# Kernel tuning notes

Hardware: AMD Instinct MI355X
Metric: run time of the kernel (lower is better)

The kernel has to match this reference:

```python
import jax, jax.numpy as jnp
import numpy as np

B, T, C_IN, C_HID, C_EMB, K, MAX_DUR = 16, 512, 512, 256, 384, 5, 8
MAX_MEL = T * MAX_DUR  # static upper bound on regulated length (4096)
LRELU_SLOPE = 0.3
PAD = (K - 1) // 2
EPS = 1e-5


def setup_inputs() -> dict:
    key = jax.random.key(0)
    ks = jax.random.split(key, 14)
    s = 0.05
    return {
        "x": jax.random.normal(ks[0], (B, T, C_IN), jnp.float32),
        "x_res": jax.random.normal(ks[1], (B, T, C_IN), jnp.float32),
        "duration_target": jax.random.randint(ks[2], (B, T), 0, MAX_DUR, dtype=jnp.int32),
        "embeddings": jax.random.normal(ks[3], (B, T, C_EMB), jnp.float32),
        "src_mask": jnp.zeros((B, T), jnp.bool_),
        "conv1_w": s * jax.random.normal(ks[4], (K, C_IN, C_HID), jnp.float32),
        "conv1_b": jnp.zeros((C_HID,), jnp.float32),
        "ln1_g": jnp.ones((C_HID,), jnp.float32),
        "ln1_b": jnp.zeros((C_HID,), jnp.float32),
        "conv2_w": s * jax.random.normal(ks[5], (K, C_HID, C_HID), jnp.float32),
        "conv2_b": jnp.zeros((C_HID,), jnp.float32),
        "ln2_g": jnp.ones((C_HID,), jnp.float32),
        "ln2_b": jnp.zeros((C_HID,), jnp.float32),
        "lin_w": s * jax.random.normal(ks[6], (C_HID, 1), jnp.float32),
        "lin_b": jnp.zeros((1,), jnp.float32),
    }


def _conv1d(x, w, b):
    # x: [B, T, Cin], w: [K, Cin, Cout] -> [B, T, Cout] (same padding)
    y = jax.lax.conv_general_dilated(
        x, w, window_strides=(1,), padding=[(PAD, PAD)],
        dimension_numbers=("NWC", "WIO", "NWC"))
    return y + b


def _layer_norm(x, g, b):
    mu = jnp.mean(x, axis=-1, keepdims=True)
    var = jnp.mean(jnp.square(x - mu), axis=-1, keepdims=True)
    return (x - mu) * jax.lax.rsqrt(var + EPS) * g + b


def _duration_predictor(x, mask, c1w, c1b, g1, b1, c2w, c2b, g2, b2, lw, lb):
    h = jax.nn.leaky_relu(_conv1d(x, c1w, c1b), LRELU_SLOPE)
    h = _layer_norm(h, g1, b1)  # dropout is identity at eval
    h = jax.nn.leaky_relu(_conv1d(h, c2w, c2b), LRELU_SLOPE)
    h = _layer_norm(h, g2, b2)
    h = (h @ lw + lb).squeeze(-1)  # [B, T]
    return jnp.where(mask, 0.0, h)


def _length_regulate(x, duration):
    # Fused prefix-sum + gather replacement for the looped expand/cat/pad.
    # token i occupies output frames [cumsum[i-1], cumsum[i])
    cum = jnp.cumsum(duration, axis=1)              # [B, T]
    total = cum[:, -1]                              # [B] mel lengths
    pos = jnp.arange(MAX_MEL, dtype=cum.dtype)      # [MAX_MEL]
    idx = jax.vmap(lambda c: jnp.searchsorted(c, pos, side="right"))(cum)  # [B, MAX_MEL]
    idx = jnp.clip(idx, 0, duration.shape[1] - 1)
    valid = (pos[None, :] < total[:, None])         # [B, MAX_MEL]
    out = jnp.take_along_axis(x, idx[..., None], axis=1)
    out = out * valid[..., None].astype(x.dtype)    # zero-padded past mel_len
    return out, total.astype(jnp.int32)


def reference(x, x_res, duration_target, embeddings, src_mask,
              conv1_w, conv1_b, ln1_g, ln1_b, conv2_w, conv2_b, ln2_g, ln2_b,
              lin_w, lin_b):
    # upsample_train path: x_res is detached before the duration predictor
    x_res = jax.lax.stop_gradient(x_res)
    log_duration_prediction = _duration_predictor(
        x_res, src_mask, conv1_w, conv1_b, ln1_g, ln1_b,
        conv2_w, conv2_b, ln2_g, ln2_b, lin_w, lin_b)
    x_up, _ = _length_regulate(x, duration_target)
    emb_up, _ = _length_regulate(embeddings, duration_target)
    return x_up, log_duration_prediction, emb_up
```

## Files before the change

### kernel.cpp

```cpp
#include <hip/hip_runtime.h>


constexpr int Bn = 16, Tn = 512, CIN1 = 512, CHID = 256, CEMB = 384, MAXMEL = 4096;
constexpr int NROWS = Bn * Tn;
#define LRELU 0.3f
#define EPSV 1e-5f

typedef __attribute__((ext_vector_type(8))) short bf16x8;
typedef __attribute__((ext_vector_type(4))) float f32x4;
typedef __attribute__((ext_vector_type(16))) float f32x16;
typedef __attribute__((ext_vector_type(4))) unsigned int u32x4;
typedef unsigned short ushort_t;

static __device__ __forceinline__ ushort_t f2bf(float f) {
  unsigned u = __builtin_bit_cast(unsigned, f);
  unsigned r = (u + 0x7fffu + ((u >> 16) & 1u)) >> 16;
  return (ushort_t)r;
}

template <int CI, bool F32IN>
static __device__ __forceinline__ void conv_body(
    int mt, int ns,
    const float* __restrict__ xin, const ushort_t* __restrict__ inbf,
    const ushort_t* __restrict__ wB, float* __restrict__ hraw) {
  constexpr int NCHUNK = CI / 128;
  constexpr int ROWS = 36, LDSTRIDE = 136;
  __shared__ ushort_t sA[ROWS * LDSTRIDE];

  const int b = mt >> 4, t0 = (mt & 15) * 32;
  const int tid = threadIdx.x;
  const int l = tid & 63, nh = tid >> 6;
  const int lm = l & 31, lq = l >> 5;
  const int cob32 = ns * 4 + nh;

  f32x16 acc;
#pragma unroll
  for (int i = 0; i < 16; ++i) acc[i] = 0.f;

  const ushort_t* pB = wB + (size_t)cob32 * 512 + l * 8;

#pragma unroll 1
  for (int chunk = 0; chunk < NCHUNK; ++chunk) {
    {
      const int cibase = chunk * 128;
#pragma unroll 1
      for (int i = 0; i < 9; ++i) {
        const int p = i * 256 + tid;
        const int r = p >> 6, c2 = (p & 63) * 2;
        const int t = t0 - 2 + r;
        unsigned hv = 0;
        if ((unsigned)t < (unsigned)Tn) {
          const size_t src = (size_t)(b * Tn + t) * CI + cibase + c2;
          if (F32IN) {
            const float2 v = *(const float2*)(xin + src);
            hv = (unsigned)f2bf(v.x) | ((unsigned)f2bf(v.y) << 16);
          } else {
            hv = *(const unsigned*)(inbf + src);
          }
        }
        const int sw = ((r >> 3) & 3) << 3;
        *(unsigned*)&sA[r * LDSTRIDE + (c2 ^ sw)] = hv;
      }
    }
    __syncthreads();

#pragma unroll 1
    for (int ksh = 0; ksh < 5; ++ksh) {
      const int r = lm + ksh;
      const int sw = ((r >> 3) & 3) << 3;
      const size_t bbase = (size_t)((ksh * (CI / 16) + chunk * 8) * 8) * 512;
#pragma unroll
      for (int kk = 0; kk < 8; ++kk) {
        const int c = (kk * 16 + lq * 8) ^ sw;
        const bf16x8 a = *(const bf16x8*)&sA[r * LDSTRIDE + c];
        const bf16x8 bv = *(const bf16x8*)(pB + bbase + (size_t)kk * 8 * 512);
        acc = __builtin_amdgcn_mfma_f32_32x32x16_bf16(a, bv, acc, 0, 0, 0);
      }
    }
    __syncthreads();
  }

  const int col = ns * 128 + nh * 32 + lm;
  float* pOut = hraw + (size_t)(b * Tn + t0) * 256 + col;
#pragma unroll
  for (int reg = 0; reg < 16; ++reg) {
    const int row = (reg & 3) + 8 * (reg >> 2) + 4 * lq;
    pOut[(size_t)row * 256] = acc[reg];
  }
}

__global__ __launch_bounds__(256, 2) void conv1_gather_kernel(
    const float* __restrict__ x_res, const ushort_t* __restrict__ w1,
    float* __restrict__ hraw,
    const float* __restrict__ x, const int* __restrict__ idx,
    float* __restrict__ x_up) {
  const int blk = blockIdx.x;
  if (blk % 3 == 0) {
    const int cid = blk / 3;
    conv_body<512, true>(cid & 255, cid >> 8, x_res, nullptr, w1, hraw);
    return;
  }
  const int gid = blk - 1 - blk / 3;
  const f32x4* x4 = (const f32x4*)x;
  f32x4* xu4 = (f32x4*)x_up;
  const int tid0 = gid * 256 + threadIdx.x;
  const int stride = 1024 * 256;
  const f32x4 z = (f32x4){0.f, 0.f, 0.f, 0.f};
  for (int u = tid0; u < Bn * MAXMEL * 128; u += stride) {
    const int bp = u >> 7, i = u & 127;
    const int t = idx[bp];
    const int b = bp >> 12;
    const f32x4 v = (t >= 0) ? x4[((b << 9) + t) * 128 + i] : z;
    __builtin_nontemporal_store(v, &xu4[u]);
  }
}

__global__ __launch_bounds__(256, 2) void conv2_gather_kernel(
    const ushort_t* __restrict__ h1, const ushort_t* __restrict__ w2,
    float* __restrict__ hraw,
    const float* __restrict__ emb, const int* __restrict__ idx,
    float* __restrict__ emb_up) {
  const int blk = blockIdx.x;
  if (blk % 3 == 0) {
    const int cid = blk / 3;
    conv_body<256, false>(cid & 255, cid >> 8, nullptr, h1, w2, hraw);
    return;
  }
  const int gid = blk - 1 - blk / 3;
  const f32x4* e4 = (const f32x4*)emb;
  f32x4* eu4 = (f32x4*)emb_up;
  const int tid0 = gid * 256 + threadIdx.x;
  const int stride = 1024 * 256;
  const f32x4 z = (f32x4){0.f, 0.f, 0.f, 0.f};
  for (int u = tid0; u < Bn * MAXMEL * 96; u += stride) {
    const int bp = u / 96, i = u - bp * 96;
    const int t = idx[bp];
    const int b = bp >> 12;
    const f32x4 v = (t >= 0) ? e4[((b << 9) + t) * 96 + i] : z;
    __builtin_nontemporal_store(v, &eu4[u]);
  }
}

template <bool FINAL>
__global__ __launch_bounds__(256) void ln_kernel(
    const float* __restrict__ hraw,
    const float* __restrict__ bias, const float* __restrict__ g,
    const float* __restrict__ be, ushort_t* __restrict__ h1,
    const float* __restrict__ lw, const float* __restrict__ lb,
    const unsigned char* __restrict__ mask, float* __restrict__ ldp) {
  const int row = blockIdx.x * 4 + (threadIdx.x >> 6);
  const int l = threadIdx.x & 63;
  const f32x4 p = ((const f32x4*)hraw)[row * 64 + l];
  const f32x4 bi = ((const f32x4*)bias)[l];
  float v0 = p.x + bi.x, v1 = p.y + bi.y, v2 = p.z + bi.z, v3 = p.w + bi.w;
  v0 = (v0 > 0.f) ? v0 : LRELU * v0;
  v1 = (v1 > 0.f) ? v1 : LRELU * v1;
  v2 = (v2 > 0.f) ? v2 : LRELU * v2;
  v3 = (v3 > 0.f) ? v3 : LRELU * v3;
  float s = v0 + v1 + v2 + v3;
  float s2 = v0 * v0 + v1 * v1 + v2 * v2 + v3 * v3;
#pragma unroll
  for (int off = 32; off >= 1; off >>= 1) {
    s += __shfl_xor(s, off);
    s2 += __shfl_xor(s2, off);
  }
  const float mu = s * (1.f / 256.f);
  const float var = s2 * (1.f / 256.f) - mu * mu;
  const float rs = rsqrtf(var + EPSV);
  const f32x4 gg = ((const f32x4*)g)[l];
  const f32x4 bb = ((const f32x4*)be)[l];
  const float h0 = (v0 - mu) * rs * gg.x + bb.x;
  const float h1v = (v1 - mu) * rs * gg.y + bb.y;
  const float h2 = (v2 - mu) * rs * gg.z + bb.z;
  const float h3 = (v3 - mu) * rs * gg.w + bb.w;
  if (!FINAL) {
    ushort4 uh;
    uh.x = f2bf(h0); uh.y = f2bf(h1v); uh.z = f2bf(h2); uh.w = f2bf(h3);
    ((ushort4*)h1)[row * 64 + l] = uh;
  } else {
    const f32x4 lv = ((const f32x4*)lw)[l];
    float d = h0 * lv.x + h1v * lv.y + h2 * lv.z + h3 * lv.w;
#pragma unroll
    for (int off = 32; off >= 1; off >>= 1) d += __shfl_xor(d, off);
    if (l == 0) {
      float val = d + lb[0];
      if (mask[row]) val = 0.f;
      ldp[row] = val;
    }
  }
}

__global__ __launch_bounds__(512) void prep_kernel(
    const float* __restrict__ w1src, const float* __restrict__ w2src,
    ushort_t* __restrict__ w1dst, ushort_t* __restrict__ w2dst,
    const int* __restrict__ dur, int* __restrict__ idx) {
  __shared__ int wsum[8];
  const int blk = blockIdx.x;
  const int tid = threadIdx.x;
  if (blk < 240) {
    const float* src;
    ushort_t* dst;
    int CI, fr, sh;
    const int wv = tid >> 6, l = tid & 63;
    if (blk < 160) { src = w1src; dst = w1dst; CI = 512; sh = 5; fr = blk * 8 + wv; }
    else           { src = w2src; dst = w2dst; CI = 256; sh = 4; fr = (blk - 160) * 8 + wv; }
    const int cob32 = fr & 7;
    const int t = fr >> 3;
    const int ksh = t >> sh;
    const int ci16 = t & ((1 << sh) - 1);
    const int ci = ci16 * 16 + (l >> 5) * 8;
    const int co = cob32 * 32 + (l & 31);
    ushort_t v[8];
#pragma unroll
    for (int j = 0; j < 8; ++j)
      v[j] = f2bf(src[((size_t)(ksh * CI + ci + j)) * 256 + co]);
    u32x4 pack;
#pragma unroll
    for (int q = 0; q < 4; ++q)
      pack[q] = (unsigned)v[q * 2] | ((unsigned)v[q * 2 + 1] << 16);
    *(u32x4*)&dst[(size_t)fr * 512 + l * 8] = pack;
    return;
  }
  const int b = blk - 240;
  const int lane = tid & 63, wv = tid >> 6;
  const int d = dur[b * Tn + tid];
  int v = d;
#pragma unroll
  for (int off = 1; off <= 32; off <<= 1) {
    const int t = __shfl_up(v, off);
    if (lane >= off) v += t;
  }
  if (lane == 63) wsum[wv] = v;
  __syncthreads();
  int woff = 0, total = 0;
#pragma unroll
  for (int i = 0; i < 8; ++i) {
    const int s = wsum[i];
    if (i < wv) woff += s;
    total += s;
  }
  const int end = v + woff;
  for (int p = end - d; p < end; ++p) idx[b * MAXMEL + p] = tid;
  for (int p = total + tid; p < MAXMEL; p += 512) idx[b * MAXMEL + p] = -1;
}

extern "C" void kernel_launch(void* const* d_in, const int* in_sizes, int n_in,
                              void* d_out, int out_size, void* d_ws, size_t ws_size,
                              hipStream_t stream) {
  const float* x     = (const float*)d_in[0];
  const float* x_res = (const float*)d_in[1];
  const int*   dur   = (const int*)d_in[2];
  const float* emb   = (const float*)d_in[3];
  const unsigned char* mask = (const unsigned char*)d_in[4];
  const float* c1w = (const float*)d_in[5];
  const float* c1b = (const float*)d_in[6];
  const float* g1  = (const float*)d_in[7];
  const float* b1  = (const float*)d_in[8];
  const float* c2w = (const float*)d_in[9];
  const float* c2b = (const float*)d_in[10];
  const float* g2  = (const float*)d_in[11];
  const float* b2  = (const float*)d_in[12];
  const float* lw  = (const float*)d_in[13];
  const float* lb  = (const float*)d_in[14];

  float* x_up   = (float*)d_out;
  float* ldp    = x_up + (size_t)Bn * MAXMEL * CIN1;
  float* emb_up = ldp + (size_t)Bn * Tn;

  int* idx = (int*)d_ws;
  ushort_t* h1 = (ushort_t*)((char*)d_ws + (size_t)Bn * MAXMEL * 4);
  ushort_t* w1 = h1 + (size_t)NROWS * 256;
  ushort_t* w2 = w1 + (size_t)5 * 512 * 256;
  float* hraw = (float*)(w2 + (size_t)5 * 256 * 256);

  prep_kernel<<<256, 512, 0, stream>>>(c1w, c2w, w1, w2, dur, idx);
  conv1_gather_kernel<<<1536, 256, 0, stream>>>(
      x_res, w1, hraw, x, idx, x_up);
  ln_kernel<false><<<NROWS / 4, 256, 0, stream>>>(
      hraw, c1b, g1, b1, h1, nullptr, nullptr, nullptr, nullptr);
  conv2_gather_kernel<<<1536, 256, 0, stream>>>(
      h1, w2, hraw, emb, idx, emb_up);
  ln_kernel<true><<<NROWS / 4, 256, 0, stream>>>(
      hraw, c2b, g2, b2, nullptr, lw, lb, mask, ldp);
}
```

Baseline: 349.6 us.

## Fuse bias, LeakyReLU and LayerNorm into conv kernels with double-buffered staging

Each conv block now covers all 256 output channels with 512 threads, so the LayerNorm epilogue (and for conv2 the final linear projection plus mask) can run in-block through shuffle and shared-memory reductions. This removes the two standalone LN kernels and the fp32 hraw round trip through global memory. The A-tile staging is double-buffered, with the next chunk's global loads issued before the MFMA loop of the current chunk. Gather blocks grow to 512 threads with fewer blocks. Trade-offs are fewer conv blocks (256 instead of 512), higher register and LDS pressure per block, and extra syncs.

```diff
diff --git a/kernel.cpp b/kernel.cpp
--- a/kernel.cpp
+++ b/kernel.cpp
@@ -18,93 +18,200 @@
   return (ushort_t)r;
 }
 
-template <int CI, bool F32IN>
-static __device__ __forceinline__ void conv_body(
-    int mt, int ns,
+template <int CI, bool F32IN, bool FINAL>
+static __device__ __forceinline__ void conv_ln_body(
+    const int mt,
     const float* __restrict__ xin, const ushort_t* __restrict__ inbf,
-    const ushort_t* __restrict__ wB, float* __restrict__ hraw) {
+    const ushort_t* __restrict__ wB,
+    const float* __restrict__ bias, const float* __restrict__ g,
+    const float* __restrict__ be, ushort_t* __restrict__ h1out,
+    const float* __restrict__ lw, const float* __restrict__ lb,
+    const unsigned char* __restrict__ mask, float* __restrict__ ldp) {
   constexpr int NCHUNK = CI / 128;
-  constexpr int ROWS = 36, LDSTRIDE = 136;
-  __shared__ ushort_t sA[ROWS * LDSTRIDE];
+  constexpr int LDSTRIDE = 136;
+  __shared__ ushort_t sA[2][36 * LDSTRIDE];
+  __shared__ float sred[32][8];
+  __shared__ float s2red[32][8];
+  __shared__ float smu[32];
+  __shared__ float srs[32];
 
   const int b = mt >> 4, t0 = (mt & 15) * 32;
   const int tid = threadIdx.x;
   const int l = tid & 63, nh = tid >> 6;
   const int lm = l & 31, lq = l >> 5;
-  const int cob32 = ns * 4 + nh;
 
   f32x16 acc;
 #pragma unroll
   for (int i = 0; i < 16; ++i) acc[i] = 0.f;
 
-  const ushort_t* pB = wB + (size_t)cob32 * 512 + l * 8;
-
-#pragma unroll 1
-  for (int chunk = 0; chunk < NCHUNK; ++chunk) {
-    {
-      const int cibase = chunk * 128;
-#pragma unroll 1
-      for (int i = 0; i < 9; ++i) {
-        const int p = i * 256 + tid;
-        const int r = p >> 6, c2 = (p & 63) * 2;
+  const ushort_t* pB = wB + (size_t)nh * 512 + l * 8;
+
+  float4 rf[3];
+  uint2 rb[3];
+
+  auto stage_load = [&](int chunk) {
+    const int cibase = chunk * 128;
+#pragma unroll
+    for (int i = 0; i < 3; ++i) {
+      const int p = i * 512 + tid;
+      if (p < 1152) {
+        const int r = p >> 5;
         const int t = t0 - 2 + r;
-        unsigned hv = 0;
         if ((unsigned)t < (unsigned)Tn) {
-          const size_t src = (size_t)(b * Tn + t) * CI + cibase + c2;
-          if (F32IN) {
-            const float2 v = *(const float2*)(xin + src);
-            hv = (unsigned)f2bf(v.x) | ((unsigned)f2bf(v.y) << 16);
+          const size_t src = (size_t)(b * Tn + t) * CI + cibase + (p & 31) * 4;
+          if constexpr (F32IN) rf[i] = *(const float4*)(xin + src);
+          else                 rb[i] = *(const uint2*)(inbf + src);
+        }
+      }
+    }
+  };
+  auto stage_write = [&](int bufi) {
+    ushort_t* sa = sA[bufi];
+#pragma unroll
+    for (int i = 0; i < 3; ++i) {
+      const int p = i * 512 + tid;
+      if (p < 1152) {
+        const int r = p >> 5, c4 = (p & 31) * 4;
+        const int t = t0 - 2 + r;
+        unsigned h0 = 0, h1v = 0;
+        if ((unsigned)t < (unsigned)Tn) {
+          if constexpr (F32IN) {
+            h0  = (unsigned)f2bf(rf[i].x) | ((unsigned)f2bf(rf[i].y) << 16);
+            h1v = (unsigned)f2bf(rf[i].z) | ((unsigned)f2bf(rf[i].w) << 16);
           } else {
-            hv = *(const unsigned*)(inbf + src);
+            h0 = rb[i].x; h1v = rb[i].y;
           }
         }
         const int sw = ((r >> 3) & 3) << 3;
-        *(unsigned*)&sA[r * LDSTRIDE + (c2 ^ sw)] = hv;
+        uint2 u; u.x = h0; u.y = h1v;
+        *(uint2*)&sa[r * LDSTRIDE + (c4 ^ sw)] = u;
       }
     }
-    __syncthreads();
-
+  };
+  auto mma_chunk = [&](int chunk, int bufi) {
+    const ushort_t* sa = sA[bufi];
 #pragma unroll 1
     for (int ksh = 0; ksh < 5; ++ksh) {
       const int r = lm + ksh;
       const int sw = ((r >> 3) & 3) << 3;
-      const size_t bbase = (size_t)((ksh * (CI / 16) + chunk * 8) * 8) * 512;
+      const ushort_t* bp2 = pB + (size_t)((ksh * (CI / 16) + chunk * 8) * 8) * 512;
 #pragma unroll
       for (int kk = 0; kk < 8; ++kk) {
         const int c = (kk * 16 + lq * 8) ^ sw;
-        const bf16x8 a = *(const bf16x8*)&sA[r * LDSTRIDE + c];
-        const bf16x8 bv = *(const bf16x8*)(pB + bbase + (size_t)kk * 8 * 512);
+        const bf16x8 a = *(const bf16x8*)&sa[r * LDSTRIDE + c];
+        const bf16x8 bv = *(const bf16x8*)(bp2 + (size_t)kk * 8 * 512);
         acc = __builtin_amdgcn_mfma_f32_32x32x16_bf16(a, bv, acc, 0, 0, 0);
       }
     }
+  };
+
+  stage_load(0);
+  stage_write(0);
+#pragma unroll 1
+  for (int c = 0; c < NCHUNK; ++c) {
     __syncthreads();
-  }
-
-  const int col = ns * 128 + nh * 32 + lm;
-  float* pOut = hraw + (size_t)(b * Tn + t0) * 256 + col;
-#pragma unroll
-  for (int reg = 0; reg < 16; ++reg) {
-    const int row = (reg & 3) + 8 * (reg >> 2) + 4 * lq;
-    pOut[(size_t)row * 256] = acc[reg];
-  }
-}
-
-__global__ __launch_bounds__(256, 2) void conv1_gather_kernel(
+    if (c + 1 < NCHUNK) stage_load(c + 1);
+    mma_chunk(c, c & 1);
+    if (c + 1 < NCHUNK) stage_write((c + 1) & 1);
+  }
+
+  const int col = nh * 32 + lm;
+  const float bi = bias[col];
+  float s[16], s2[16];
+#pragma unroll
+  for (int rg = 0; rg < 16; ++rg) {
+    float xv = acc[rg] + bi;
+    xv = (xv > 0.f) ? xv : LRELU * xv;
+    acc[rg] = xv;
+    s[rg] = xv;
+    s2[rg] = xv * xv;
+  }
+#pragma unroll
+  for (int off = 16; off >= 1; off >>= 1) {
+#pragma unroll
+    for (int rg = 0; rg < 16; ++rg) {
+      s[rg]  += __shfl_xor(s[rg], off);
+      s2[rg] += __shfl_xor(s2[rg], off);
+    }
+  }
+  if (lm == 0) {
+#pragma unroll
+    for (int rg = 0; rg < 16; ++rg) {
+      const int row = (rg & 3) + 8 * (rg >> 2) + 4 * lq;
+      sred[row][nh] = s[rg];
+      s2red[row][nh] = s2[rg];
+    }
+  }
+  __syncthreads();
+  if (tid < 32) {
+    float a = 0.f, q = 0.f;
+#pragma unroll
+    for (int w = 0; w < 8; ++w) { a += sred[tid][w]; q += s2red[tid][w]; }
+    const float mu = a * (1.f / 256.f);
+    const float var = q * (1.f / 256.f) - mu * mu;
+    smu[tid] = mu;
+    srs[tid] = rsqrtf(var + EPSV);
+  }
+  __syncthreads();
+
+  const float gc = g[col], bc = be[col];
+  if constexpr (!FINAL) {
+    ushort_t* po = h1out + (size_t)(b * Tn + t0) * 256 + col;
+#pragma unroll
+    for (int rg = 0; rg < 16; ++rg) {
+      const int row = (rg & 3) + 8 * (rg >> 2) + 4 * lq;
+      const float h = (acc[rg] - smu[row]) * srs[row] * gc + bc;
+      po[(size_t)row * 256] = f2bf(h);
+    }
+  } else {
+    const float wc = lw[col];
+    float d[16];
+#pragma unroll
+    for (int rg = 0; rg < 16; ++rg) {
+      const int row = (rg & 3) + 8 * (rg >> 2) + 4 * lq;
+      const float h = (acc[rg] - smu[row]) * srs[row] * gc + bc;
+      d[rg] = h * wc;
+    }
+#pragma unroll
+    for (int off = 16; off >= 1; off >>= 1) {
+#pragma unroll
+      for (int rg = 0; rg < 16; ++rg) d[rg] += __shfl_xor(d[rg], off);
+    }
+    if (lm == 0) {
+#pragma unroll
+      for (int rg = 0; rg < 16; ++rg) {
+        const int row = (rg & 3) + 8 * (rg >> 2) + 4 * lq;
+        sred[row][nh] = d[rg];
+      }
+    }
+    __syncthreads();
+    if (tid < 32) {
+      float a = lb[0];
+#pragma unroll
+      for (int w = 0; w < 8; ++w) a += sred[tid][w];
+      const int grow = b * Tn + t0 + tid;
+      ldp[grow] = mask[grow] ? 0.f : a;
+    }
+  }
+}
+
+__global__ __launch_bounds__(512, 4) void conv1_fused_kernel(
     const float* __restrict__ x_res, const ushort_t* __restrict__ w1,
-    float* __restrict__ hraw,
+    const float* __restrict__ c1b, const float* __restrict__ g1,
+    const float* __restrict__ b1, ushort_t* __restrict__ h1,
     const float* __restrict__ x, const int* __restrict__ idx,
     float* __restrict__ x_up) {
   const int blk = blockIdx.x;
   if (blk % 3 == 0) {
-    const int cid = blk / 3;
-    conv_body<512, true>(cid & 255, cid >> 8, x_res, nullptr, w1, hraw);
+    conv_ln_body<512, true, false>(blk / 3, x_res, nullptr, w1, c1b, g1, b1, h1,
+                                   nullptr, nullptr, nullptr, nullptr);
     return;
   }
   const int gid = blk - 1 - blk / 3;
   const f32x4* x4 = (const f32x4*)x;
   f32x4* xu4 = (f32x4*)x_up;
-  const int tid0 = gid * 256 + threadIdx.x;
-  const int stride = 1024 * 256;
+  const int tid0 = gid * 512 + threadIdx.x;
+  const int stride = 512 * 512;
   const f32x4 z = (f32x4){0.f, 0.f, 0.f, 0.f};
   for (int u = tid0; u < Bn * MAXMEL * 128; u += stride) {
     const int bp = u >> 7, i = u & 127;
@@ -115,22 +222,25 @@
   }
 }
 
-__global__ __launch_bounds__(256, 2) void conv2_gather_kernel(
+__global__ __launch_bounds__(512, 4) void conv2_fused_kernel(
     const ushort_t* __restrict__ h1, const ushort_t* __restrict__ w2,
-    float* __restrict__ hraw,
+    const float* __restrict__ c2b, const float* __restrict__ g2,
+    const float* __restrict__ b2, const float* __restrict__ lw,
+    const float* __restrict__ lb, const unsigned char* __restrict__ mask,
+    float* __restrict__ ldp,
     const float* __restrict__ emb, const int* __restrict__ idx,
     float* __restrict__ emb_up) {
   const int blk = blockIdx.x;
   if (blk % 3 == 0) {
-    const int cid = blk / 3;
-    conv_body<256, false>(cid & 255, cid >> 8, nullptr, h1, w2, hraw);
+    conv_ln_body<256, false, true>(blk / 3, nullptr, h1, w2, c2b, g2, b2,
+                                   nullptr, lw, lb, mask, ldp);
     return;
   }
   const int gid = blk - 1 - blk / 3;
   const f32x4* e4 = (const f32x4*)emb;
   f32x4* eu4 = (f32x4*)emb_up;
-  const int tid0 = gid * 256 + threadIdx.x;
-  const int stride = 1024 * 256;
+  const int tid0 = gid * 512 + threadIdx.x;
+  const int stride = 512 * 512;
   const f32x4 z = (f32x4){0.f, 0.f, 0.f, 0.f};
   for (int u = tid0; u < Bn * MAXMEL * 96; u += stride) {
     const int bp = u / 96, i = u - bp * 96;
@@ -138,55 +248,6 @@
     const int b = bp >> 12;
     const f32x4 v = (t >= 0) ? e4[((b << 9) + t) * 96 + i] : z;
     __builtin_nontemporal_store(v, &eu4[u]);
-  }
-}
-
-template <bool FINAL>
-__global__ __launch_bounds__(256) void ln_kernel(
-    const float* __restrict__ hraw,
-    const float* __restrict__ bias, const float* __restrict__ g,
-    const float* __restrict__ be, ushort_t* __restrict__ h1,
-    const float* __restrict__ lw, const float* __restrict__ lb,
-    const unsigned char* __restrict__ mask, float* __restrict__ ldp) {
-  const int row = blockIdx.x * 4 + (threadIdx.x >> 6);
-  const int l = threadIdx.x & 63;
-  const f32x4 p = ((const f32x4*)hraw)[row * 64 + l];
-  const f32x4 bi = ((const f32x4*)bias)[l];
-  float v0 = p.x + bi.x, v1 = p.y + bi.y, v2 = p.z + bi.z, v3 = p.w + bi.w;
-  v0 = (v0 > 0.f) ? v0 : LRELU * v0;
-  v1 = (v1 > 0.f) ? v1 : LRELU * v1;
-  v2 = (v2 > 0.f) ? v2 : LRELU * v2;
-  v3 = (v3 > 0.f) ? v3 : LRELU * v3;
-  float s = v0 + v1 + v2 + v3;
-  float s2 = v0 * v0 + v1 * v1 + v2 * v2 + v3 * v3;
-#pragma unroll
-  for (int off = 32; off >= 1; off >>= 1) {
-    s += __shfl_xor(s, off);
-    s2 += __shfl_xor(s2, off);
-  }
-  const float mu = s * (1.f / 256.f);
-  const float var = s2 * (1.f / 256.f) - mu * mu;
-  const float rs = rsqrtf(var + EPSV);
-  const f32x4 gg = ((const f32x4*)g)[l];
-  const f32x4 bb = ((const f32x4*)be)[l];
-  const float h0 = (v0 - mu) * rs * gg.x + bb.x;
-  const float h1v = (v1 - mu) * rs * gg.y + bb.y;
-  const float h2 = (v2 - mu) * rs * gg.z + bb.z;
-  const float h3 = (v3 - mu) * rs * gg.w + bb.w;
-  if (!FINAL) {
-    ushort4 uh;
-    uh.x = f2bf(h0); uh.y = f2bf(h1v); uh.z = f2bf(h2); uh.w = f2bf(h3);
-    ((ushort4*)h1)[row * 64 + l] = uh;
-  } else {
-    const f32x4 lv = ((const f32x4*)lw)[l];
-    float d = h0 * lv.x + h1v * lv.y + h2 * lv.z + h3 * lv.w;
-#pragma unroll
-    for (int off = 32; off >= 1; off >>= 1) d += __shfl_xor(d, off);
-    if (l == 0) {
-      float val = d + lb[0];
-      if (mask[row]) val = 0.f;
-      ldp[row] = val;
-    }
   }
 }
 
@@ -271,15 +332,10 @@
   ushort_t* h1 = (ushort_t*)((char*)d_ws + (size_t)Bn * MAXMEL * 4);
   ushort_t* w1 = h1 + (size_t)NROWS * 256;
   ushort_t* w2 = w1 + (size_t)5 * 512 * 256;
-  float* hraw = (float*)(w2 + (size_t)5 * 256 * 256);
 
   prep_kernel<<<256, 512, 0, stream>>>(c1w, c2w, w1, w2, dur, idx);
-  conv1_gather_kernel<<<1536, 256, 0, stream>>>(
-      x_res, w1, hraw, x, idx, x_up);
-  ln_kernel<false><<<NROWS / 4, 256, 0, stream>>>(
-      hraw, c1b, g1, b1, h1, nullptr, nullptr, nullptr, nullptr);
-  conv2_gather_kernel<<<1536, 256, 0, stream>>>(
-      h1, w2, hraw, emb, idx, emb_up);
-  ln_kernel<true><<<NROWS / 4, 256, 0, stream>>>(
-      hraw, c2b, g2, b2, nullptr, lw, lb, mask, ldp);
-}
+  conv1_fused_kernel<<<768, 512, 0, stream>>>(
+      x_res, w1, c1b, g1, b1, h1, x, idx, x_up);
+  conv2_fused_kernel<<<768, 512, 0, stream>>>(
+      h1, w2, c2b, g2, b2, lw, lb, mask, ldp, emb, idx, emb_up);
+}
```

Result: slower. 361.9 us (+3.5%).

## Fuse conv2 with LayerNorm2 and projection; pair LN1 with embedding gather

Applied to the files above, without the earlier changes.

Conv2 is now computed by a dedicated kernel in which each block handles 32 time rows across all 256 output channels. Bias, LeakyReLU, LayerNorm and the final linear projection are applied in-register with cross-wave reductions through shared memory, so the fp32 conv2 result never round-trips through global memory. The first LayerNorm moves into the kernel that also performs the embedding gather, removing one launch and letting that memory-bound copy overlap with the LN work. The cost is that conv2 now runs alone on only 256 blocks with no gather work to overlap, which may leave much of the GPU idle.

```diff
diff --git a/kernel.cpp b/kernel.cpp
--- a/kernel.cpp
+++ b/kernel.cpp
@@ -115,18 +115,45 @@
   }
 }
 
-__global__ __launch_bounds__(256, 2) void conv2_gather_kernel(
-    const ushort_t* __restrict__ h1, const ushort_t* __restrict__ w2,
-    float* __restrict__ hraw,
+__global__ __launch_bounds__(256, 2) void ln1_emb_kernel(
+    const float* __restrict__ hraw,
+    const float* __restrict__ bias, const float* __restrict__ g,
+    const float* __restrict__ be, ushort_t* __restrict__ h1,
     const float* __restrict__ emb, const int* __restrict__ idx,
     float* __restrict__ emb_up) {
   const int blk = blockIdx.x;
-  if (blk % 3 == 0) {
-    const int cid = blk / 3;
-    conv_body<256, false>(cid & 255, cid >> 8, nullptr, h1, w2, hraw);
+  if (blk % 3 != 2) {
+    const int lid = (blk / 3) * 2 + (blk % 3);
+    const int row = lid * 4 + (threadIdx.x >> 6);
+    const int l = threadIdx.x & 63;
+    const f32x4 p = ((const f32x4*)hraw)[row * 64 + l];
+    const f32x4 bi = ((const f32x4*)bias)[l];
+    float v0 = p.x + bi.x, v1 = p.y + bi.y, v2 = p.z + bi.z, v3 = p.w + bi.w;
+    v0 = (v0 > 0.f) ? v0 : LRELU * v0;
+    v1 = (v1 > 0.f) ? v1 : LRELU * v1;
+    v2 = (v2 > 0.f) ? v2 : LRELU * v2;
+    v3 = (v3 > 0.f) ? v3 : LRELU * v3;
+    float s = v0 + v1 + v2 + v3;
+    float s2 = v0 * v0 + v1 * v1 + v2 * v2 + v3 * v3;
+#pragma unroll
+    for (int off = 32; off >= 1; off >>= 1) {
+      s += __shfl_xor(s, off);
+      s2 += __shfl_xor(s2, off);
+    }
+    const float mu = s * (1.f / 256.f);
+    const float var = s2 * (1.f / 256.f) - mu * mu;
+    const float rs = rsqrtf(var + EPSV);
+    const f32x4 gg = ((const f32x4*)g)[l];
+    const f32x4 bb = ((const f32x4*)be)[l];
+    ushort4 uh;
+    uh.x = f2bf((v0 - mu) * rs * gg.x + bb.x);
+    uh.y = f2bf((v1 - mu) * rs * gg.y + bb.y);
+    uh.z = f2bf((v2 - mu) * rs * gg.z + bb.z);
+    uh.w = f2bf((v3 - mu) * rs * gg.w + bb.w);
+    ((ushort4*)h1)[row * 64 + l] = uh;
     return;
   }
-  const int gid = blk - 1 - blk / 3;
+  const int gid = blk / 3;
   const f32x4* e4 = (const f32x4*)emb;
   f32x4* eu4 = (f32x4*)emb_up;
   const int tid0 = gid * 256 + threadIdx.x;
@@ -141,52 +168,146 @@
   }
 }
 
-template <bool FINAL>
-__global__ __launch_bounds__(256) void ln_kernel(
-    const float* __restrict__ hraw,
-    const float* __restrict__ bias, const float* __restrict__ g,
-    const float* __restrict__ be, ushort_t* __restrict__ h1,
-    const float* __restrict__ lw, const float* __restrict__ lb,
-    const unsigned char* __restrict__ mask, float* __restrict__ ldp) {
-  const int row = blockIdx.x * 4 + (threadIdx.x >> 6);
-  const int l = threadIdx.x & 63;
-  const f32x4 p = ((const f32x4*)hraw)[row * 64 + l];
-  const f32x4 bi = ((const f32x4*)bias)[l];
-  float v0 = p.x + bi.x, v1 = p.y + bi.y, v2 = p.z + bi.z, v3 = p.w + bi.w;
-  v0 = (v0 > 0.f) ? v0 : LRELU * v0;
-  v1 = (v1 > 0.f) ? v1 : LRELU * v1;
-  v2 = (v2 > 0.f) ? v2 : LRELU * v2;
-  v3 = (v3 > 0.f) ? v3 : LRELU * v3;
-  float s = v0 + v1 + v2 + v3;
-  float s2 = v0 * v0 + v1 * v1 + v2 * v2 + v3 * v3;
-#pragma unroll
-  for (int off = 32; off >= 1; off >>= 1) {
-    s += __shfl_xor(s, off);
-    s2 += __shfl_xor(s2, off);
-  }
-  const float mu = s * (1.f / 256.f);
-  const float var = s2 * (1.f / 256.f) - mu * mu;
-  const float rs = rsqrtf(var + EPSV);
-  const f32x4 gg = ((const f32x4*)g)[l];
-  const f32x4 bb = ((const f32x4*)be)[l];
-  const float h0 = (v0 - mu) * rs * gg.x + bb.x;
-  const float h1v = (v1 - mu) * rs * gg.y + bb.y;
-  const float h2 = (v2 - mu) * rs * gg.z + bb.z;
-  const float h3 = (v3 - mu) * rs * gg.w + bb.w;
-  if (!FINAL) {
-    ushort4 uh;
-    uh.x = f2bf(h0); uh.y = f2bf(h1v); uh.z = f2bf(h2); uh.w = f2bf(h3);
-    ((ushort4*)h1)[row * 64 + l] = uh;
-  } else {
-    const f32x4 lv = ((const f32x4*)lw)[l];
-    float d = h0 * lv.x + h1v * lv.y + h2 * lv.z + h3 * lv.w;
-#pragma unroll
-    for (int off = 32; off >= 1; off >>= 1) d += __shfl_xor(d, off);
-    if (l == 0) {
-      float val = d + lb[0];
-      if (mask[row]) val = 0.f;
-      ldp[row] = val;
-    }
+__global__ __launch_bounds__(256, 2) void conv2_fused_kernel(
+    const ushort_t* __restrict__ h1, const ushort_t* __restrict__ w2,
+    const float* __restrict__ c2b, const float* __restrict__ g2,
+    const float* __restrict__ b2, const float* __restrict__ lw,
+    const float* __restrict__ lb, const unsigned char* __restrict__ mask,
+    float* __restrict__ ldp) {
+  constexpr int CI = 256;
+  constexpr int ROWS = 36, LDSTRIDE = 136;
+  __shared__ ushort_t sA[ROWS * LDSTRIDE];
+  __shared__ float sred[32][4];
+  __shared__ float s2red[32][4];
+  __shared__ float smu[32];
+  __shared__ float srs[32];
+
+  const int mt = blockIdx.x;
+  const int b = mt >> 4, t0 = (mt & 15) * 32;
+  const int tid = threadIdx.x;
+  const int l = tid & 63, nh = tid >> 6;
+  const int lm = l & 31, lq = l >> 5;
+
+  f32x16 acc0, acc1;
+#pragma unroll
+  for (int i = 0; i < 16; ++i) { acc0[i] = 0.f; acc1[i] = 0.f; }
+
+  const ushort_t* pB0 = w2 + (size_t)nh * 512 + l * 8;
+  const ushort_t* pB1 = w2 + (size_t)(nh + 4) * 512 + l * 8;
+
+#pragma unroll 1
+  for (int chunk = 0; chunk < 2; ++chunk) {
+    {
+      const int cibase = chunk * 128;
+#pragma unroll 1
+      for (int i = 0; i < 9; ++i) {
+        const int p = i * 256 + tid;
+        const int r = p >> 6, c2 = (p & 63) * 2;
+        const int t = t0 - 2 + r;
+        unsigned hv = 0;
+        if ((unsigned)t < (unsigned)Tn) {
+          const size_t src = (size_t)(b * Tn + t) * CI + cibase + c2;
+          hv = *(const unsigned*)(h1 + src);
+        }
+        const int sw = ((r >> 3) & 3) << 3;
+        *(unsigned*)&sA[r * LDSTRIDE + (c2 ^ sw)] = hv;
+      }
+    }
+    __syncthreads();
+
+#pragma unroll 1
+    for (int ksh = 0; ksh < 5; ++ksh) {
+      const int r = lm + ksh;
+      const int sw = ((r >> 3) & 3) << 3;
+      const size_t bbase = (size_t)((ksh * (CI / 16) + chunk * 8) * 8) * 512;
+#pragma unroll
+      for (int kk = 0; kk < 8; ++kk) {
+        const int c = (kk * 16 + lq * 8) ^ sw;
+        const bf16x8 a = *(const bf16x8*)&sA[r * LDSTRIDE + c];
+        const bf16x8 bv0 = *(const bf16x8*)(pB0 + bbase + (size_t)kk * 8 * 512);
+        const bf16x8 bv1 = *(const bf16x8*)(pB1 + bbase + (size_t)kk * 8 * 512);
+        acc0 = __builtin_amdgcn_mfma_f32_32x32x16_bf16(a, bv0, acc0, 0, 0, 0);
+        acc1 = __builtin_amdgcn_mfma_f32_32x32x16_bf16(a, bv1, acc1, 0, 0, 0);
+      }
+    }
+    __syncthreads();
+  }
+
+  const int col0 = nh * 32 + lm;
+  const int col1 = col0 + 128;
+  const float bi0 = c2b[col0], bi1 = c2b[col1];
+  float s[16], s2v[16];
+#pragma unroll
+  for (int rg = 0; rg < 16; ++rg) {
+    float a0 = acc0[rg] + bi0;
+    float a1 = acc1[rg] + bi1;
+    a0 = (a0 > 0.f) ? a0 : LRELU * a0;
+    a1 = (a1 > 0.f) ? a1 : LRELU * a1;
+    acc0[rg] = a0;
+    acc1[rg] = a1;
+    s[rg] = a0 + a1;
+    s2v[rg] = a0 * a0 + a1 * a1;
+  }
+#pragma unroll
+  for (int off = 16; off >= 1; off >>= 1) {
+#pragma unroll
+    for (int rg = 0; rg < 16; ++rg) {
+      s[rg] += __shfl_xor(s[rg], off);
+      s2v[rg] += __shfl_xor(s2v[rg], off);
+    }
+  }
+  if (lm == 0) {
+#pragma unroll
+    for (int rg = 0; rg < 16; ++rg) {
+      const int row = (rg & 3) + 8 * (rg >> 2) + 4 * lq;
+      sred[row][nh] = s[rg];
+      s2red[row][nh] = s2v[rg];
+    }
+  }
+  __syncthreads();
+  if (tid < 32) {
+    float a = 0.f, q = 0.f;
+#pragma unroll
+    for (int w = 0; w < 4; ++w) { a += sred[tid][w]; q += s2red[tid][w]; }
+    const float mu = a * (1.f / 256.f);
+    const float var = q * (1.f / 256.f) - mu * mu;
+    smu[tid] = mu;
+    srs[tid] = rsqrtf(var + EPSV);
+  }
+  __syncthreads();
+
+  const float g0 = g2[col0], g1v = g2[col1];
+  const float be0 = b2[col0], be1 = b2[col1];
+  const float w0 = lw[col0], w1v = lw[col1];
+  float d[16];
+#pragma unroll
+  for (int rg = 0; rg < 16; ++rg) {
+    const int row = (rg & 3) + 8 * (rg >> 2) + 4 * lq;
+    const float mu = smu[row], rs = srs[row];
+    const float h0 = (acc0[rg] - mu) * rs * g0 + be0;
+    const float h1v = (acc1[rg] - mu) * rs * g1v + be1;
+    d[rg] = h0 * w0 + h1v * w1v;
+  }
+#pragma unroll
+  for (int off = 16; off >= 1; off >>= 1) {
+#pragma unroll
+    for (int rg = 0; rg < 16; ++rg) d[rg] += __shfl_xor(d[rg], off);
+  }
+  __syncthreads();
+  if (lm == 0) {
+#pragma unroll
+    for (int rg = 0; rg < 16; ++rg) {
+      const int row = (rg & 3) + 8 * (rg >> 2) + 4 * lq;
+      sred[row][nh] = d[rg];
+    }
+  }
+  __syncthreads();
+  if (tid < 32) {
+    float a = lb[0];
+#pragma unroll
+    for (int w = 0; w < 4; ++w) a += sred[tid][w];
+    const int grow = b * Tn + t0 + tid;
+    ldp[grow] = mask[grow] ? 0.f : a;
   }
 }
 
@@ -276,10 +397,8 @@
   prep_kernel<<<256, 512, 0, stream>>>(c1w, c2w, w1, w2, dur, idx);
   conv1_gather_kernel<<<1536, 256, 0, stream>>>(
       x_res, w1, hraw, x, idx, x_up);
-  ln_kernel<false><<<NROWS / 4, 256, 0, stream>>>(
-      hraw, c1b, g1, b1, h1, nullptr, nullptr, nullptr, nullptr);
-  conv2_gather_kernel<<<1536, 256, 0, stream>>>(
-      h1, w2, hraw, emb, idx, emb_up);
-  ln_kernel<true><<<NROWS / 4, 256, 0, stream>>>(
-      hraw, c2b, g2, b2, nullptr, lw, lb, mask, ldp);
-}
+  ln1_emb_kernel<<<3072, 256, 0, stream>>>(
+      hraw, c1b, g1, b1, h1, emb, idx, emb_up);
+  conv2_fused_kernel<<<256, 256, 0, stream>>>(
+      h1, w2, c2b, g2, b2, lw, lb, mask, ldp);
+}
```

Result: slower. 364.6 us (+4.3%).
